# Optimization experiments

Measured on AMD Instinct MI355X. Metric: run time of the kernel, lower is better.

Reference implementation:

```python
import jax, jax.numpy as jnp
import numpy as np

EPS = 1e-6

def _layer_norm(x, w, b):
    mu = jnp.mean(x, axis=-1, keepdims=True)
    var = jnp.mean((x - mu) ** 2, axis=-1, keepdims=True)
    return (x - mu) * jax.lax.rsqrt(var + EPS) * w + b

def setup_inputs() -> dict:
    key = jax.random.key(0)
    ks = jax.random.split(key, 8)
    B, N, C = 4, 1024, 2048
    H = C * 2  # mlp hidden = 2*feature_dim
    std = 0.01
    x = jax.random.normal(ks[0], (B, N, C), dtype=jnp.float32)
    wq = jax.random.normal(ks[1], (C, C), dtype=jnp.float32) * std
    wk = jax.random.normal(ks[2], (C, C), dtype=jnp.float32) * std
    wv = jax.random.normal(ks[3], (C, C), dtype=jnp.float32) * std
    ln1_w = jnp.ones((C,), jnp.float32); ln1_b = jnp.zeros((C,), jnp.float32)
    fc1_w = jax.random.normal(ks[4], (H, C), dtype=jnp.float32) * std
    fc1_b = jnp.zeros((H,), jnp.float32)
    fc2_w = jax.random.normal(ks[5], (C, H), dtype=jnp.float32) * std
    fc2_b = jnp.zeros((C,), jnp.float32)
    ln2_w = jnp.ones((C,), jnp.float32); ln2_b = jnp.zeros((C,), jnp.float32)
    return {"x": x, "wq": wq, "wk": wk, "wv": wv,
            "ln1_w": ln1_w, "ln1_b": ln1_b,
            "fc1_w": fc1_w, "fc1_b": fc1_b,
            "fc2_w": fc2_w, "fc2_b": fc2_b,
            "ln2_w": ln2_w, "ln2_b": ln2_b}

def reference(x, wq, wk, wv, ln1_w, ln1_b, fc1_w, fc1_b, fc2_w, fc2_b, ln2_w, ln2_b):
    B, N, C = x.shape
    num_head = 32
    d = C // num_head
    # QKV projections (no bias), split heads: [B, H, N, d]
    def proj(w):
        return (x @ w.T).reshape(B, N, num_head, d).transpose(0, 2, 1, 3)
    q, k, v = proj(wq), proj(wk), proj(wv)
    scale = 1.0 / jnp.sqrt(jnp.float32(d))
    attn = jnp.einsum('bhnd,bhmd->bhnm', q * scale, k)
    attn = jax.nn.softmax(attn, axis=-1)
    out = jnp.einsum('bhnm,bhmd->bhnd', attn, v)
    out = out.transpose(0, 2, 1, 3).reshape(B, N, C)
    out = _layer_norm(out + x, ln1_w, ln1_b)
    # MLP with residual + post-LN
    h = jax.nn.relu(out @ fc1_w.T + fc1_b)
    h = h @ fc2_w.T + fc2_b
    out = _layer_norm(out + h, ln2_w, ln2_b)
    return out
```

## Files before the change

kernel.cpp:

```cpp
#include <hip/hip_runtime.h>

#define C_DIM   2048
#define H_DIM   4096
#define NSEQ    1024
#define NBATCH  4
#define BN_ROWS 4096
#define NHEAD   32
#define DHEAD   64

typedef __attribute__((ext_vector_type(8))) short  short8;
typedef __attribute__((ext_vector_type(4))) float  f32x4;

__device__ __forceinline__ float bf2f(unsigned short u) {
    union { unsigned int i; float f; } v; v.i = ((unsigned int)u) << 16; return v.f;
}
__device__ __forceinline__ unsigned short f2bf(float f) {
    union { float f; unsigned int i; } v; v.f = f;
    unsigned int r = v.i + 0x7fffu + ((v.i >> 16) & 1u);
    return (unsigned short)(r >> 16);
}

#define G2L16(gp, lp) \
    __builtin_amdgcn_global_load_lds((const __attribute__((address_space(1))) void*)(gp), \
                                     (__attribute__((address_space(3))) void*)(lp), 16, 0, 0)

__global__ __launch_bounds__(256)
void cvt_all(const float* __restrict__ x,   unsigned short* __restrict__ xo,
             const float* __restrict__ w0,  unsigned short* __restrict__ w0o,
             const float* __restrict__ w1,  unsigned short* __restrict__ w1o,
             const float* __restrict__ w2,  unsigned short* __restrict__ w2o,
             const float* __restrict__ w3,  unsigned short* __restrict__ w3o,
             const float* __restrict__ w4,  unsigned short* __restrict__ w4o)
{
    int bid = blockIdx.x;
    const float* src; unsigned short* dst;
    if      (bid < 4096)  { src = x;  dst = xo;  }
    else if (bid < 6144)  { src = w0; dst = w0o; bid -= 4096;  }
    else if (bid < 8192)  { src = w1; dst = w1o; bid -= 6144;  }
    else if (bid < 10240) { src = w2; dst = w2o; bid -= 8192;  }
    else if (bid < 14336) { src = w3; dst = w3o; bid -= 10240; }
    else                  { src = w4; dst = w4o; bid -= 14336; }
    const size_t i = ((size_t)bid * 256 + threadIdx.x) * 8;
    float4 a = *(const float4*)(src + i);
    float4 b = *(const float4*)(src + i + 4);
    unsigned short o[8] = { f2bf(a.x), f2bf(a.y), f2bf(a.z), f2bf(a.w),
                            f2bf(b.x), f2bf(b.y), f2bf(b.z), f2bf(b.w) };
    *(int4*)(dst + i) = *(const int4*)o;
}

template<int EPI, typename OUT_T>
__global__ __launch_bounds__(256)
void gemm_ring(const unsigned short* __restrict__ A,
               const unsigned short* __restrict__ B,
               const float* __restrict__ bias,
               OUT_T* __restrict__ C, int M, int N, int K)
{
    __shared__ unsigned short As[4][128 * 32];
    __shared__ unsigned short Bs[4][128 * 32];

    const int t    = threadIdx.x;
    const int lane = t & 63;
    const int wave = t >> 6;
    const int m0 = blockIdx.x * 128, n0 = blockIdx.y * 128;
    const int wm = (wave >> 1) * 64, wn = (wave & 1) * 64;
    const int lr = lane & 15;
    const int kq = lane >> 4;
    const int lrow = lane >> 2;
    const int lcol = (lane & 3) * 8;
    const int NT = K >> 5;

    const int arow = m0 + wave * 32 + lrow;
    const int brow = n0 + wave * 32 + lrow;
    const int rb   = wave * 32;

    f32x4 acc[4][4] = {};

#define STAGE_T(slot, ktile) do {                                              \
    const int koff_ = (ktile) * 32 + lcol;                                     \
    G2L16(&A[(size_t)(arow)      * K + koff_], &As[slot][ rb       * 32]);     \
    G2L16(&A[(size_t)(arow + 16) * K + koff_], &As[slot][(rb + 16) * 32]);     \
    G2L16(&B[(size_t)(brow)      * K + koff_], &Bs[slot][ rb       * 32]);     \
    G2L16(&B[(size_t)(brow + 16) * K + koff_], &Bs[slot][(rb + 16) * 32]);     \
  } while (0)

    STAGE_T(0, 0);
    STAGE_T(1, 1);
    STAGE_T(2, 2);

    for (int kt = 0; kt < NT; ++kt) {
        if (kt < NT - 2)       asm volatile("s_waitcnt vmcnt(8)" ::: "memory");
        else if (kt == NT - 2) asm volatile("s_waitcnt vmcnt(4)" ::: "memory");
        else                   asm volatile("s_waitcnt vmcnt(0)" ::: "memory");
        __builtin_amdgcn_s_barrier();

        const int s = kt & 3;
        short8 af[4], bf[4];
        #pragma unroll
        for (int i = 0; i < 4; ++i)
            af[i] = *(const short8*)&As[s][(wm + i * 16 + lr) * 32 + kq * 8];
        #pragma unroll
        for (int j = 0; j < 4; ++j)
            bf[j] = *(const short8*)&Bs[s][(wn + j * 16 + lr) * 32 + kq * 8];
        #pragma unroll
        for (int i = 0; i < 4; ++i)
            #pragma unroll
            for (int j = 0; j < 4; ++j)
                acc[i][j] = __builtin_amdgcn_mfma_f32_16x16x32_bf16(af[i], bf[j], acc[i][j], 0, 0, 0);

        if (kt + 3 < NT) STAGE_T((kt + 3) & 3, kt + 3);
    }

    #pragma unroll
    for (int j = 0; j < 4; ++j) {
        const int col = n0 + wn + j * 16 + lr;
        float bv = 0.f;
        if (EPI > 0) bv = bias[col];
        #pragma unroll
        for (int i = 0; i < 4; ++i) {
            #pragma unroll
            for (int r = 0; r < 4; ++r) {
                const int row = m0 + wm + i * 16 + kq * 4 + r;
                float v = acc[i][j][r] + bv;
                if (EPI == 1) v = fmaxf(v, 0.f);
                if constexpr (sizeof(OUT_T) == 2) C[(size_t)row * N + col] = f2bf(v);
                else                              C[(size_t)row * N + col] = v;
            }
        }
    }
#undef STAGE_T
}

__global__ __launch_bounds__(256)
void gemm_qkv(const unsigned short* __restrict__ A,
              const unsigned short* __restrict__ Wq,
              const unsigned short* __restrict__ Wk,
              const unsigned short* __restrict__ Wv,
              unsigned short* __restrict__ Qo,
              unsigned short* __restrict__ Ko,
              unsigned short* __restrict__ Vo)
{
    __shared__ unsigned short As[4][128 * 32];
    __shared__ unsigned short Bs[4][128 * 32];

    const int t    = threadIdx.x;
    const int lane = t & 63;
    const int wave = t >> 6;
    const int m0 = blockIdx.x * 128;
    const int ng = blockIdx.y * 128;
    const unsigned short* B; unsigned short* Cp; int n0;
    if      (ng < 2048) { B = Wq; Cp = Qo; n0 = ng; }
    else if (ng < 4096) { B = Wk; Cp = Ko; n0 = ng - 2048; }
    else                { B = Wv; Cp = Vo; n0 = ng - 4096; }

    const int wm = (wave >> 1) * 64, wn = (wave & 1) * 64;
    const int lr = lane & 15;
    const int kq = lane >> 4;
    const int lrow = lane >> 2;
    const int lcol = (lane & 3) * 8;
    const int NT = C_DIM >> 5;

    const int arow = m0 + wave * 32 + lrow;
    const int brow = n0 + wave * 32 + lrow;
    const int rb   = wave * 32;

    f32x4 acc[4][4] = {};

#define STAGE_T(slot, ktile) do {                                                   \
    const int koff_ = (ktile) * 32 + lcol;                                          \
    G2L16(&A[(size_t)(arow)      * C_DIM + koff_], &As[slot][ rb       * 32]);      \
    G2L16(&A[(size_t)(arow + 16) * C_DIM + koff_], &As[slot][(rb + 16) * 32]);      \
    G2L16(&B[(size_t)(brow)      * C_DIM + koff_], &Bs[slot][ rb       * 32]);      \
    G2L16(&B[(size_t)(brow + 16) * C_DIM + koff_], &Bs[slot][(rb + 16) * 32]);      \
  } while (0)

    STAGE_T(0, 0);
    STAGE_T(1, 1);
    STAGE_T(2, 2);

    for (int kt = 0; kt < NT; ++kt) {
        if (kt < NT - 2)       asm volatile("s_waitcnt vmcnt(8)" ::: "memory");
        else if (kt == NT - 2) asm volatile("s_waitcnt vmcnt(4)" ::: "memory");
        else                   asm volatile("s_waitcnt vmcnt(0)" ::: "memory");
        __builtin_amdgcn_s_barrier();

        const int s = kt & 3;
        short8 af[4], bf[4];
        #pragma unroll
        for (int i = 0; i < 4; ++i)
            af[i] = *(const short8*)&As[s][(wm + i * 16 + lr) * 32 + kq * 8];
        #pragma unroll
        for (int j = 0; j < 4; ++j)
            bf[j] = *(const short8*)&Bs[s][(wn + j * 16 + lr) * 32 + kq * 8];
        #pragma unroll
        for (int i = 0; i < 4; ++i)
            #pragma unroll
            for (int j = 0; j < 4; ++j)
                acc[i][j] = __builtin_amdgcn_mfma_f32_16x16x32_bf16(af[i], bf[j], acc[i][j], 0, 0, 0);

        if (kt + 3 < NT) STAGE_T((kt + 3) & 3, kt + 3);
    }

    #pragma unroll
    for (int j = 0; j < 4; ++j) {
        const int col = n0 + wn + j * 16 + lr;
        #pragma unroll
        for (int i = 0; i < 4; ++i) {
            #pragma unroll
            for (int r = 0; r < 4; ++r) {
                const int row = m0 + wm + i * 16 + kq * 4 + r;
                Cp[(size_t)row * C_DIM + col] = f2bf(acc[i][j][r]);
            }
        }
    }
#undef STAGE_T
}

#define LDK 72
__global__ __launch_bounds__(256)
void attn_mfma(const unsigned short* __restrict__ Qg,
               const unsigned short* __restrict__ Kg,
               const unsigned short* __restrict__ Vg,
               unsigned short* __restrict__ Og)
{
    __shared__ unsigned short Ks[64 * LDK];
    __shared__ unsigned short Vt[64 * LDK];
    __shared__ unsigned short Ps[64 * LDK];

    const int t    = threadIdx.x;
    const int lane = t & 63;
    const int wave = t >> 6;
    const int lr   = lane & 15;
    const int quad = lane >> 4;
    const int bh = blockIdx.y;
    const int b  = bh >> 5, h = bh & 31;
    const int q0 = blockIdx.x * 64;
    const int colbase = h * 64;

    short8 qf[2];
    {
        const size_t qrow = (size_t)(b * NSEQ + q0 + wave * 16 + lr) * C_DIM + colbase;
        #pragma unroll
        for (int kc = 0; kc < 2; ++kc) {
            short8 raw = *(const short8*)(Qg + qrow + kc * 32 + quad * 8);
            short8 sc;
            #pragma unroll
            for (int j = 0; j < 8; ++j)
                sc[j] = (short)f2bf(bf2f((unsigned short)raw[j]) * 0.125f);
            qf[kc] = sc;
        }
    }

    f32x4 Oacc[4] = {};
    float li[4] = {};

    for (int kt = 0; kt < 16; ++kt) {
        __syncthreads();
        {
            const int r = t >> 2, sg = (t & 3) * 16;
            const size_t grow = (size_t)(b * NSEQ + kt * 64 + r) * C_DIM + colbase + sg;
            *(int4*)&Ks[r * LDK + sg]     = *(const int4*)(Kg + grow);
            *(int4*)&Ks[r * LDK + sg + 8] = *(const int4*)(Kg + grow + 8);
        }
        {
            const int key = t & 63, d0 = (t >> 6) * 16;
            const size_t grow = (size_t)(b * NSEQ + kt * 64 + key) * C_DIM + colbase + d0;
            int4 u0 = *(const int4*)(Vg + grow);
            int4 u1 = *(const int4*)(Vg + grow + 8);
            const unsigned short* us0 = (const unsigned short*)&u0;
            const unsigned short* us1 = (const unsigned short*)&u1;
            #pragma unroll
            for (int j = 0; j < 8; ++j) {
                Vt[(d0 + j)     * LDK + key] = us0[j];
                Vt[(d0 + j + 8) * LDK + key] = us1[j];
            }
        }
        __syncthreads();

        f32x4 s[4] = {};
        #pragma unroll
        for (int n = 0; n < 4; ++n)
            #pragma unroll
            for (int kc = 0; kc < 2; ++kc) {
                short8 kf = *(const short8*)&Ks[(n * 16 + lr) * LDK + kc * 32 + quad * 8];
                s[n] = __builtin_amdgcn_mfma_f32_16x16x32_bf16(qf[kc], kf, s[n], 0, 0, 0);
            }

        float p[4][4];
        #pragma unroll
        for (int r = 0; r < 4; ++r) {
            #pragma unroll
            for (int n = 0; n < 4; ++n) { p[n][r] = __expf(s[n][r]); }
            li[r] += p[0][r] + p[1][r] + p[2][r] + p[3][r];
        }

        #pragma unroll
        for (int r = 0; r < 4; ++r)
            #pragma unroll
            for (int n = 0; n < 4; ++n)
                Ps[(wave * 16 + quad * 4 + r) * LDK + n * 16 + lr] = f2bf(p[n][r]);

        short8 pf[2];
        #pragma unroll
        for (int kc = 0; kc < 2; ++kc)
            pf[kc] = *(const short8*)&Ps[(wave * 16 + lr) * LDK + kc * 32 + quad * 8];

        #pragma unroll
        for (int n = 0; n < 4; ++n)
            #pragma unroll
            for (int kc = 0; kc < 2; ++kc) {
                short8 vf = *(const short8*)&Vt[(n * 16 + lr) * LDK + kc * 32 + quad * 8];
                Oacc[n] = __builtin_amdgcn_mfma_f32_16x16x32_bf16(pf[kc], vf, Oacc[n], 0, 0, 0);
            }
    }

    #pragma unroll
    for (int r = 0; r < 4; ++r) {
        #pragma unroll
        for (int off = 1; off < 16; off <<= 1) li[r] += __shfl_xor(li[r], off, 64);
        const float inv = 1.f / li[r];
        const size_t rowb = (size_t)(b * NSEQ + q0 + wave * 16 + quad * 4 + r) * C_DIM + colbase;
        #pragma unroll
        for (int n = 0; n < 4; ++n)
            Og[rowb + n * 16 + lr] = f2bf(Oacc[n][r] * inv);
    }
}

__global__ __launch_bounds__(256)
void ln_fused1(const unsigned short* __restrict__ a, const float* __restrict__ xr,
               const float* __restrict__ w, const float* __restrict__ bb,
               unsigned short* __restrict__ y16)
{
    const int row = blockIdx.x, t = threadIdx.x;
    const size_t base = (size_t)row * C_DIM;
    const int c0 = t * 8;
    float v[8];
    int4 ai = *(const int4*)(a + base + c0);
    const unsigned short* as = (const unsigned short*)&ai;
    float4 x0 = *(const float4*)(xr + base + c0);
    float4 x1 = *(const float4*)(xr + base + c0 + 4);
    v[0] = bf2f(as[0]) + x0.x; v[1] = bf2f(as[1]) + x0.y;
    v[2] = bf2f(as[2]) + x0.z; v[3] = bf2f(as[3]) + x0.w;
    v[4] = bf2f(as[4]) + x1.x; v[5] = bf2f(as[5]) + x1.y;
    v[6] = bf2f(as[6]) + x1.z; v[7] = bf2f(as[7]) + x1.w;

    float s = 0.f, s2 = 0.f;
    #pragma unroll
    for (int k = 0; k < 8; ++k) { s += v[k]; s2 += v[k] * v[k]; }
    #pragma unroll
    for (int off = 32; off; off >>= 1) { s += __shfl_xor(s, off, 64); s2 += __shfl_xor(s2, off, 64); }
    __shared__ float red[8];
    if ((t & 63) == 0) { red[t >> 6] = s; red[4 + (t >> 6)] = s2; }
    __syncthreads();
    s  = red[0] + red[1] + red[2] + red[3];
    s2 = red[4] + red[5] + red[6] + red[7];
    const float mu = s * (1.f / C_DIM);
    const float rs = rsqrtf(s2 * (1.f / C_DIM) - mu * mu + 1e-6f);

    float4 w0 = *(const float4*)(w + c0);
    float4 w1 = *(const float4*)(w + c0 + 4);
    float4 b0 = *(const float4*)(bb + c0);
    float4 b1 = *(const float4*)(bb + c0 + 4);
    const float* wf = (const float*)&w0; const float* wg = (const float*)&w1;
    const float* bf = (const float*)&b0; const float* bg = (const float*)&b1;
    unsigned short o16[8];
    #pragma unroll
    for (int k = 0; k < 4; ++k) {
        o16[k]     = f2bf((v[k]     - mu) * rs * wf[k] + bf[k]);
        o16[k + 4] = f2bf((v[k + 4] - mu) * rs * wg[k] + bg[k]);
    }
    *(int4*)(y16 + base + c0) = *(const int4*)o16;
}

__global__ __launch_bounds__(256)
void ln_fused2(const unsigned short* __restrict__ a, const unsigned short* __restrict__ b2,
               const float* __restrict__ w, const float* __restrict__ bb,
               float* __restrict__ out)
{
    const int row = blockIdx.x, t = threadIdx.x;
    const size_t base = (size_t)row * C_DIM;
    const int c0 = t * 8;
    float v[8];
    int4 ai = *(const int4*)(a + base + c0);
    int4 bi = *(const int4*)(b2 + base + c0);
    const unsigned short* as = (const unsigned short*)&ai;
    const unsigned short* bs = (const unsigned short*)&bi;
    #pragma unroll
    for (int k = 0; k < 8; ++k) v[k] = bf2f(as[k]) + bf2f(bs[k]);

    float s = 0.f, s2 = 0.f;
    #pragma unroll
    for (int k = 0; k < 8; ++k) { s += v[k]; s2 += v[k] * v[k]; }
    #pragma unroll
    for (int off = 32; off; off >>= 1) { s += __shfl_xor(s, off, 64); s2 += __shfl_xor(s2, off, 64); }
    __shared__ float red[8];
    if ((t & 63) == 0) { red[t >> 6] = s; red[4 + (t >> 6)] = s2; }
    __syncthreads();
    s  = red[0] + red[1] + red[2] + red[3];
    s2 = red[4] + red[5] + red[6] + red[7];
    const float mu = s * (1.f / C_DIM);
    const float rs = rsqrtf(s2 * (1.f / C_DIM) - mu * mu + 1e-6f);

    float4 w0 = *(const float4*)(w + c0);
    float4 w1 = *(const float4*)(w + c0 + 4);
    float4 b0 = *(const float4*)(bb + c0);
    float4 b1 = *(const float4*)(bb + c0 + 4);
    const float* wf = (const float*)&w0; const float* wg = (const float*)&w1;
    const float* bf = (const float*)&b0; const float* bg = (const float*)&b1;
    float4 o0, o1;
    #pragma unroll
    for (int k = 0; k < 4; ++k) {
        ((float*)&o0)[k] = (v[k]     - mu) * rs * wf[k] + bf[k];
        ((float*)&o1)[k] = (v[k + 4] - mu) * rs * wg[k] + bg[k];
    }
    *(float4*)(out + base + c0)     = o0;
    *(float4*)(out + base + c0 + 4) = o1;
}

extern "C" void kernel_launch(void* const* d_in, const int* in_sizes, int n_in,
                              void* d_out, int out_size, void* d_ws, size_t ws_size,
                              hipStream_t stream)
{
    (void)in_sizes; (void)n_in; (void)out_size; (void)ws_size;
    const float* x    = (const float*)d_in[0];
    const float* wq   = (const float*)d_in[1];
    const float* wk   = (const float*)d_in[2];
    const float* wv   = (const float*)d_in[3];
    const float* ln1w = (const float*)d_in[4];
    const float* ln1b = (const float*)d_in[5];
    const float* fc1w = (const float*)d_in[6];
    const float* fc1b = (const float*)d_in[7];
    const float* fc2w = (const float*)d_in[8];
    const float* fc2b = (const float*)d_in[9];
    const float* ln2w = (const float*)d_in[10];
    const float* ln2b = (const float*)d_in[11];

    char* ws = (char*)d_ws;
    const size_t MB16 = (size_t)BN_ROWS * C_DIM * 2;
    unsigned short* xb    = (unsigned short*)(ws);
    unsigned short* attnb = (unsigned short*)(ws);
    unsigned short* wqb   = (unsigned short*)(ws + MB16);
    unsigned short* wkb   = (unsigned short*)(ws + MB16 + MB16 / 2);
    unsigned short* y16   = (unsigned short*)(ws + MB16);
    unsigned short* wvb   = (unsigned short*)(ws + 2 * MB16);
    unsigned short* fc1wb = (unsigned short*)(ws + 2 * MB16 + MB16 / 2);
    unsigned short* fc2wb = (unsigned short*)(ws + 3 * MB16 + MB16 / 2);
    unsigned short* q_ws  = (unsigned short*)(ws + 4 * MB16 + MB16 / 2);
    unsigned short* h2    = (unsigned short*)(ws + 4 * MB16 + MB16 / 2);
    unsigned short* k_ws  = (unsigned short*)(ws + 5 * MB16 + MB16 / 2);
    unsigned short* v_ws  = (unsigned short*)(ws + 6 * MB16 + MB16 / 2);
    unsigned short* hbuf  = (unsigned short*)(ws + 5 * MB16 + MB16 / 2);

    dim3 blk(256);

    cvt_all<<<dim3(18432), blk, 0, stream>>>(x, xb, wq, wqb, wk, wkb, wv, wvb,
                                             fc1w, fc1wb, fc2w, fc2wb);

    gemm_qkv<<<dim3(32, 48), blk, 0, stream>>>(xb, wqb, wkb, wvb, q_ws, k_ws, v_ws);
    attn_mfma<<<dim3(NSEQ / 64, NBATCH * NHEAD), blk, 0, stream>>>(q_ws, k_ws, v_ws, attnb);
    ln_fused1<<<dim3(BN_ROWS), blk, 0, stream>>>(attnb, x, ln1w, ln1b, y16);
    gemm_ring<1, unsigned short><<<dim3(32, 32), blk, 0, stream>>>(y16, fc1wb, fc1b, hbuf, BN_ROWS, H_DIM, C_DIM);
    gemm_ring<2, unsigned short><<<dim3(32, 16), blk, 0, stream>>>(hbuf, fc2wb, fc2b, h2, BN_ROWS, C_DIM, H_DIM);
    ln_fused2<<<dim3(BN_ROWS), blk, 0, stream>>>(y16, h2, ln2w, ln2b, (float*)d_out);
}
```

Before: 580.9 us.

## Use 256x256-tile 8-wave GEMM with swizzled LDS for QKV and FC1

Adds a new GEMM body with 256x256 output tiles, 512 threads (8 waves), K-tile of 64, double-buffered LDS filled by direct global-to-LDS loads, and an XOR swizzle to avoid bank conflicts. It interleaves staged loads with MFMA quarter-steps and raises wave priority around the MFMA blocks. QKV and FC1 now use it instead of the 128x128 ring kernel. Larger tiles raise arithmetic intensity and cut global traffic. The costs are 128KB of LDS per block, fewer blocks (256 to 384) for 256 CUs, and many barriers per K step.

```diff
diff --git a/kernel.cpp b/kernel.cpp
--- a/kernel.cpp
+++ b/kernel.cpp
@@ -48,6 +48,167 @@
     *(int4*)(dst + i) = *(const int4*)o;
 }
 
+template<int EPI>
+__device__ __forceinline__
+void gemm256_body(const unsigned short* __restrict__ A,
+                  const unsigned short* __restrict__ B,
+                  const float* __restrict__ bias,
+                  unsigned short* __restrict__ C,
+                  const int m0, const int n0, const int K, const int ldc)
+{
+    __shared__ unsigned short As[2][256 * 64];
+    __shared__ unsigned short Bs[2][256 * 64];
+
+    const int t  = threadIdx.x;
+    const int l  = t & 63;
+    const int w  = t >> 6;
+    const int wr = w >> 2;
+    const int wc = w & 3;
+    const int lr = l & 15;
+    const int kq = l >> 4;
+    const int slotA = lr & 7;
+
+    const int sr = l >> 3;
+    const int sg = ((l & 7) ^ sr) * 8;
+
+    f32x4 acc[8][4] = {};
+    short8 bf[4][2], af[2][2];
+
+#define STG(src, srow0, ktile, ldsdst) do {                                         \
+    const unsigned short* gp0_ = (src) + (size_t)((srow0) + w * 8 + sr) * K         \
+                                  + (ktile) * 64 + sg;                              \
+    const unsigned short* gp1_ = (src) + (size_t)((srow0) + 64 + w * 8 + sr) * K    \
+                                  + (ktile) * 64 + sg;                              \
+    G2L16(gp0_, (ldsdst) + (w * 8) * 64);                                           \
+    G2L16(gp1_, (ldsdst) + (64 + w * 8) * 64);                                      \
+  } while (0)
+
+#define LDB(buf) do {                                                               \
+    _Pragma("unroll") for (int n_ = 0; n_ < 4; ++n_)                                \
+      _Pragma("unroll") for (int ks_ = 0; ks_ < 2; ++ks_)                           \
+        bf[n_][ks_] = *(const short8*)&Bs[buf][                                     \
+            (wc * 64 + n_ * 16 + lr) * 64 + (((ks_ << 2) | kq) ^ slotA) * 8];       \
+  } while (0)
+
+#define LDA(buf, q) do {                                                            \
+    _Pragma("unroll") for (int i_ = 0; i_ < 2; ++i_)                                \
+      _Pragma("unroll") for (int ks_ = 0; ks_ < 2; ++ks_)                           \
+        af[i_][ks_] = *(const short8*)&As[buf][                                     \
+            (wr * 128 + ((q) * 2 + i_) * 16 + lr) * 64                              \
+            + (((ks_ << 2) | kq) ^ slotA) * 8];                                     \
+  } while (0)
+
+#define MM(q) do {                                                                  \
+    __builtin_amdgcn_s_setprio(1);                                                  \
+    _Pragma("unroll") for (int i_ = 0; i_ < 2; ++i_)                                \
+      _Pragma("unroll") for (int n_ = 0; n_ < 4; ++n_)                              \
+        _Pragma("unroll") for (int ks_ = 0; ks_ < 2; ++ks_)                         \
+          acc[(q) * 2 + i_][n_] = __builtin_amdgcn_mfma_f32_16x16x32_bf16(          \
+              af[i_][ks_], bf[n_][ks_], acc[(q) * 2 + i_][n_], 0, 0, 0);            \
+    __builtin_amdgcn_s_setprio(0);                                                  \
+  } while (0)
+
+#define BARR() __builtin_amdgcn_s_barrier()
+#define WLG0() asm volatile("s_waitcnt lgkmcnt(0)" ::: "memory")
+
+    const int NT = K >> 6;
+    const int IT = NT >> 1;
+
+    STG(B, n0,       0, &Bs[0][0]);
+    STG(B, n0 + 128, 0, &Bs[0][128 * 64]);
+    STG(A, m0,       0, &As[0][0]);
+    STG(A, m0 + 128, 0, &As[0][128 * 64]);
+    STG(B, n0,       1, &Bs[1][0]);
+    STG(B, n0 + 128, 1, &Bs[1][128 * 64]);
+    asm volatile("s_waitcnt vmcnt(4)" ::: "memory");
+    BARR();
+
+    for (int it = 0; it < IT; ++it) {
+        const int T1 = 2 * it + 1, T2 = 2 * it + 2, T3 = 2 * it + 3;
+        const bool haveT2 = (T2 < NT), haveT3 = (T3 < NT);
+
+        LDB(0); LDA(0, 0);
+        STG(A, m0, T1, &As[1][0]);
+        BARR(); WLG0(); MM(0); BARR();
+        LDA(0, 1);
+        STG(A, m0 + 128, T1, &As[1][128 * 64]);
+        BARR(); WLG0(); MM(1); BARR();
+        LDA(0, 2);
+        if (haveT2) STG(B, n0, T2, &Bs[0][0]);
+        BARR(); WLG0(); MM(2); BARR();
+        LDA(0, 3);
+        if (haveT2) STG(B, n0 + 128, T2, &Bs[0][128 * 64]);
+        BARR(); WLG0(); MM(3);
+        if (haveT2) asm volatile("s_waitcnt vmcnt(4)" ::: "memory");
+        else        asm volatile("s_waitcnt vmcnt(0)" ::: "memory");
+        BARR();
+        LDB(1); LDA(1, 0);
+        if (haveT2) STG(A, m0, T2, &As[0][0]);
+        BARR(); WLG0(); MM(0); BARR();
+        LDA(1, 1);
+        if (haveT2) STG(A, m0 + 128, T2, &As[0][128 * 64]);
+        BARR(); WLG0(); MM(1); BARR();
+        LDA(1, 2);
+        if (haveT3) STG(B, n0, T3, &Bs[1][0]);
+        BARR(); WLG0(); MM(2); BARR();
+        LDA(1, 3);
+        if (haveT3) STG(B, n0 + 128, T3, &Bs[1][128 * 64]);
+        BARR(); WLG0(); MM(3);
+        if (it + 1 < IT) asm volatile("s_waitcnt vmcnt(4)" ::: "memory");
+        BARR();
+    }
+
+    #pragma unroll
+    for (int n = 0; n < 4; ++n) {
+        const int col = n0 + wc * 64 + n * 16 + lr;
+        float bv = 0.f;
+        if (EPI > 0) bv = bias[col];
+        #pragma unroll
+        for (int m = 0; m < 8; ++m) {
+            #pragma unroll
+            for (int r = 0; r < 4; ++r) {
+                const int row = m0 + wr * 128 + m * 16 + kq * 4 + r;
+                float v = acc[m][n][r] + bv;
+                if (EPI == 1) v = fmaxf(v, 0.f);
+                C[(size_t)row * ldc + col] = f2bf(v);
+            }
+        }
+    }
+#undef STG
+#undef LDB
+#undef LDA
+#undef MM
+#undef BARR
+#undef WLG0
+}
+
+__global__ __launch_bounds__(512, 2)
+void gemm256_fc1(const unsigned short* __restrict__ A,
+                 const unsigned short* __restrict__ B,
+                 const float* __restrict__ bias,
+                 unsigned short* __restrict__ C)
+{
+    gemm256_body<1>(A, B, bias, C, blockIdx.x * 256, blockIdx.y * 256, C_DIM, H_DIM);
+}
+
+__global__ __launch_bounds__(512, 2)
+void gemm256_qkv(const unsigned short* __restrict__ A,
+                 const unsigned short* __restrict__ Wq,
+                 const unsigned short* __restrict__ Wk,
+                 const unsigned short* __restrict__ Wv,
+                 unsigned short* __restrict__ Qo,
+                 unsigned short* __restrict__ Ko,
+                 unsigned short* __restrict__ Vo)
+{
+    const int by = blockIdx.y;
+    const unsigned short* B; unsigned short* Cp;
+    if      (by < 8)  { B = Wq; Cp = Qo; }
+    else if (by < 16) { B = Wk; Cp = Ko; }
+    else              { B = Wv; Cp = Vo; }
+    const int n0 = (by & 7) * 256;
+    gemm256_body<0>(A, B, nullptr, Cp, blockIdx.x * 256, n0, C_DIM, C_DIM);
+}
+
 template<int EPI, typename OUT_T>
 __global__ __launch_bounds__(256)
 void gemm_ring(const unsigned short* __restrict__ A,
@@ -94,18 +255,18 @@
         __builtin_amdgcn_s_barrier();
 
         const int s = kt & 3;
-        short8 af[4], bf[4];
+        short8 af[4], bfr[4];
         #pragma unroll
         for (int i = 0; i < 4; ++i)
             af[i] = *(const short8*)&As[s][(wm + i * 16 + lr) * 32 + kq * 8];
         #pragma unroll
         for (int j = 0; j < 4; ++j)
-            bf[j] = *(const short8*)&Bs[s][(wn + j * 16 + lr) * 32 + kq * 8];
+            bfr[j] = *(const short8*)&Bs[s][(wn + j * 16 + lr) * 32 + kq * 8];
         #pragma unroll
         for (int i = 0; i < 4; ++i)
             #pragma unroll
             for (int j = 0; j < 4; ++j)
-                acc[i][j] = __builtin_amdgcn_mfma_f32_16x16x32_bf16(af[i], bf[j], acc[i][j], 0, 0, 0);
+                acc[i][j] = __builtin_amdgcn_mfma_f32_16x16x32_bf16(af[i], bfr[j], acc[i][j], 0, 0, 0);
 
         if (kt + 3 < NT) STAGE_T((kt + 3) & 3, kt + 3);
     }
@@ -124,91 +285,6 @@
                 if (EPI == 1) v = fmaxf(v, 0.f);
                 if constexpr (sizeof(OUT_T) == 2) C[(size_t)row * N + col] = f2bf(v);
                 else                              C[(size_t)row * N + col] = v;
-            }
-        }
-    }
-#undef STAGE_T
-}
-
-__global__ __launch_bounds__(256)
-void gemm_qkv(const unsigned short* __restrict__ A,
-              const unsigned short* __restrict__ Wq,
-              const unsigned short* __restrict__ Wk,
-              const unsigned short* __restrict__ Wv,
-              unsigned short* __restrict__ Qo,
-              unsigned short* __restrict__ Ko,
-              unsigned short* __restrict__ Vo)
-{
-    __shared__ unsigned short As[4][128 * 32];
-    __shared__ unsigned short Bs[4][128 * 32];
-
-    const int t    = threadIdx.x;
-    const int lane = t & 63;
-    const int wave = t >> 6;
-    const int m0 = blockIdx.x * 128;
-    const int ng = blockIdx.y * 128;
-    const unsigned short* B; unsigned short* Cp; int n0;
-    if      (ng < 2048) { B = Wq; Cp = Qo; n0 = ng; }
-    else if (ng < 4096) { B = Wk; Cp = Ko; n0 = ng - 2048; }
-    else                { B = Wv; Cp = Vo; n0 = ng - 4096; }
-
-    const int wm = (wave >> 1) * 64, wn = (wave & 1) * 64;
-    const int lr = lane & 15;
-    const int kq = lane >> 4;
-    const int lrow = lane >> 2;
-    const int lcol = (lane & 3) * 8;
-    const int NT = C_DIM >> 5;
-
-    const int arow = m0 + wave * 32 + lrow;
-    const int brow = n0 + wave * 32 + lrow;
-    const int rb   = wave * 32;
-
-    f32x4 acc[4][4] = {};
-
-#define STAGE_T(slot, ktile) do {                                                   \
-    const int koff_ = (ktile) * 32 + lcol;                                          \
-    G2L16(&A[(size_t)(arow)      * C_DIM + koff_], &As[slot][ rb       * 32]);      \
-    G2L16(&A[(size_t)(arow + 16) * C_DIM + koff_], &As[slot][(rb + 16) * 32]);      \
-    G2L16(&B[(size_t)(brow)      * C_DIM + koff_], &Bs[slot][ rb       * 32]);      \
-    G2L16(&B[(size_t)(brow + 16) * C_DIM + koff_], &Bs[slot][(rb + 16) * 32]);      \
-  } while (0)
-
-    STAGE_T(0, 0);
-    STAGE_T(1, 1);
-    STAGE_T(2, 2);
-
-    for (int kt = 0; kt < NT; ++kt) {
-        if (kt < NT - 2)       asm volatile("s_waitcnt vmcnt(8)" ::: "memory");
-        else if (kt == NT - 2) asm volatile("s_waitcnt vmcnt(4)" ::: "memory");
-        else                   asm volatile("s_waitcnt vmcnt(0)" ::: "memory");
-        __builtin_amdgcn_s_barrier();
-
-        const int s = kt & 3;
-        short8 af[4], bf[4];
-        #pragma unroll
-        for (int i = 0; i < 4; ++i)
-            af[i] = *(const short8*)&As[s][(wm + i * 16 + lr) * 32 + kq * 8];
-        #pragma unroll
-        for (int j = 0; j < 4; ++j)
-            bf[j] = *(const short8*)&Bs[s][(wn + j * 16 + lr) * 32 + kq * 8];
-        #pragma unroll
-        for (int i = 0; i < 4; ++i)
-            #pragma unroll
-            for (int j = 0; j < 4; ++j)
-                acc[i][j] = __builtin_amdgcn_mfma_f32_16x16x32_bf16(af[i], bf[j], acc[i][j], 0, 0, 0);
-
-        if (kt + 3 < NT) STAGE_T((kt + 3) & 3, kt + 3);
-    }
-
-    #pragma unroll
-    for (int j = 0; j < 4; ++j) {
-        const int col = n0 + wn + j * 16 + lr;
-        #pragma unroll
-        for (int i = 0; i < 4; ++i) {
-            #pragma unroll
-            for (int r = 0; r < 4; ++r) {
-                const int row = m0 + wm + i * 16 + kq * 4 + r;
-                Cp[(size_t)row * C_DIM + col] = f2bf(acc[i][j][r]);
             }
         }
     }
@@ -256,10 +332,10 @@
     for (int kt = 0; kt < 16; ++kt) {
         __syncthreads();
         {
-            const int r = t >> 2, sg = (t & 3) * 16;
-            const size_t grow = (size_t)(b * NSEQ + kt * 64 + r) * C_DIM + colbase + sg;
-            *(int4*)&Ks[r * LDK + sg]     = *(const int4*)(Kg + grow);
-            *(int4*)&Ks[r * LDK + sg + 8] = *(const int4*)(Kg + grow + 8);
+            const int r = t >> 2, sg2 = (t & 3) * 16;
+            const size_t grow = (size_t)(b * NSEQ + kt * 64 + r) * C_DIM + colbase + sg2;
+            *(int4*)&Ks[r * LDK + sg2]     = *(const int4*)(Kg + grow);
+            *(int4*)&Ks[r * LDK + sg2 + 8] = *(const int4*)(Kg + grow + 8);
         }
         {
             const int key = t & 63, d0 = (t >> 6) * 16;
@@ -455,10 +531,10 @@
     cvt_all<<<dim3(18432), blk, 0, stream>>>(x, xb, wq, wqb, wk, wkb, wv, wvb,
                                              fc1w, fc1wb, fc2w, fc2wb);
 
-    gemm_qkv<<<dim3(32, 48), blk, 0, stream>>>(xb, wqb, wkb, wvb, q_ws, k_ws, v_ws);
+    gemm256_qkv<<<dim3(16, 24), dim3(512), 0, stream>>>(xb, wqb, wkb, wvb, q_ws, k_ws, v_ws);
     attn_mfma<<<dim3(NSEQ / 64, NBATCH * NHEAD), blk, 0, stream>>>(q_ws, k_ws, v_ws, attnb);
     ln_fused1<<<dim3(BN_ROWS), blk, 0, stream>>>(attnb, x, ln1w, ln1b, y16);
-    gemm_ring<1, unsigned short><<<dim3(32, 32), blk, 0, stream>>>(y16, fc1wb, fc1b, hbuf, BN_ROWS, H_DIM, C_DIM);
+    gemm256_fc1<<<dim3(16, 16), dim3(512), 0, stream>>>(y16, fc1wb, fc1b, hbuf);
     gemm_ring<2, unsigned short><<<dim3(32, 16), blk, 0, stream>>>(hbuf, fc2wb, fc2b, h2, BN_ROWS, C_DIM, H_DIM);
     ln_fused2<<<dim3(BN_ROWS), blk, 0, stream>>>(y16, h2, ln2w, ln2b, (float*)d_out);
 }
```

Result: no change. 588.7 us (+1.3%).

## Write V transposed from QKV GEMM and load V fragments directly in attention

Applied to the files above, without the earlier changes.

The QKV GEMM now writes V in transposed [C, B*N] layout, so the attention kernel loads V fragments straight from global memory into registers. This drops the per-tile LDS transpose of V and its scalar shared-memory stores. The QKV GEMM is also rewritten without the 4-stage ring pipeline: it uses a single LDS buffer with two syncthreads per k-tile, which exposes global-load latency. The transposed V stores are 8-byte scattered writes at large stride.

```diff
diff --git a/kernel.cpp b/kernel.cpp
--- a/kernel.cpp
+++ b/kernel.cpp
@@ -9,6 +9,7 @@
 #define DHEAD   64
 
 typedef __attribute__((ext_vector_type(8))) short  short8;
+typedef __attribute__((ext_vector_type(4))) short  short4v;
 typedef __attribute__((ext_vector_type(4))) float  f32x4;
 
 __device__ __forceinline__ float bf2f(unsigned short u) {
@@ -48,6 +49,90 @@
     *(int4*)(dst + i) = *(const int4*)o;
 }
 
+__global__ __launch_bounds__(256)
+void gemm_qkv(const unsigned short* __restrict__ A,
+              const unsigned short* __restrict__ Wq,
+              const unsigned short* __restrict__ Wk,
+              const unsigned short* __restrict__ Wv,
+              unsigned short* __restrict__ Qo,
+              unsigned short* __restrict__ Ko,
+              unsigned short* __restrict__ Vo)
+{
+    __shared__ unsigned short As[128 * 32];
+    __shared__ unsigned short Bs[128 * 32];
+
+    const int t    = threadIdx.x;
+    const int lane = t & 63;
+    const int wave = t >> 6;
+    const int m0 = blockIdx.x * 128;
+    const int ng = blockIdx.y * 128;
+    const unsigned short* B; unsigned short* Cp; int n0; bool vtrans = false;
+    if      (ng < 2048) { B = Wq; Cp = Qo; n0 = ng; }
+    else if (ng < 4096) { B = Wk; Cp = Ko; n0 = ng - 2048; }
+    else                { B = Wv; Cp = Vo; n0 = ng - 4096; vtrans = true; }
+
+    const int wm = (wave >> 1) * 64, wn = (wave & 1) * 64;
+    const int lr = lane & 15;
+    const int kq = lane >> 4;
+
+    f32x4 acc[4][4] = {};
+
+    const int lrow = lane >> 2;
+    const int lcol = (lane & 3) * 8;
+
+    for (int kt = 0; kt < C_DIM; kt += 32) {
+        __syncthreads();
+        #pragma unroll
+        for (int p = 0; p < 2; ++p) {
+            const int rb = wave * 32 + p * 16;
+            G2L16(&A[(size_t)(m0 + rb + lrow) * C_DIM + kt + lcol], &As[rb * 32]);
+            G2L16(&B[(size_t)(n0 + rb + lrow) * C_DIM + kt + lcol], &Bs[rb * 32]);
+        }
+        __syncthreads();
+
+        short8 af[4], bf[4];
+        #pragma unroll
+        for (int i = 0; i < 4; ++i)
+            af[i] = *(const short8*)&As[(wm + i * 16 + lr) * 32 + kq * 8];
+        #pragma unroll
+        for (int j = 0; j < 4; ++j)
+            bf[j] = *(const short8*)&Bs[(wn + j * 16 + lr) * 32 + kq * 8];
+        #pragma unroll
+        for (int i = 0; i < 4; ++i)
+            #pragma unroll
+            for (int j = 0; j < 4; ++j)
+                acc[i][j] = __builtin_amdgcn_mfma_f32_16x16x32_bf16(af[i], bf[j], acc[i][j], 0, 0, 0);
+    }
+
+    if (!vtrans) {
+        #pragma unroll
+        for (int j = 0; j < 4; ++j) {
+            const int col = n0 + wn + j * 16 + lr;
+            #pragma unroll
+            for (int i = 0; i < 4; ++i) {
+                #pragma unroll
+                for (int r = 0; r < 4; ++r) {
+                    const int row = m0 + wm + i * 16 + kq * 4 + r;
+                    Cp[(size_t)row * C_DIM + col] = f2bf(acc[i][j][r]);
+                }
+            }
+        }
+    } else {
+        #pragma unroll
+        for (int j = 0; j < 4; ++j) {
+            const int col = n0 + wn + j * 16 + lr;
+            #pragma unroll
+            for (int i = 0; i < 4; ++i) {
+                const int row0 = m0 + wm + i * 16 + kq * 4;
+                short4v o4;
+                #pragma unroll
+                for (int r = 0; r < 4; ++r) o4[r] = (short)f2bf(acc[i][j][r]);
+                *(short4v*)&Vo[(size_t)col * BN_ROWS + row0] = o4;
+            }
+        }
+    }
+}
+
 template<int EPI, typename OUT_T>
 __global__ __launch_bounds__(256)
 void gemm_ring(const unsigned short* __restrict__ A,
@@ -94,18 +179,18 @@
         __builtin_amdgcn_s_barrier();
 
         const int s = kt & 3;
-        short8 af[4], bf[4];
+        short8 af[4], bfr[4];
         #pragma unroll
         for (int i = 0; i < 4; ++i)
             af[i] = *(const short8*)&As[s][(wm + i * 16 + lr) * 32 + kq * 8];
         #pragma unroll
         for (int j = 0; j < 4; ++j)
-            bf[j] = *(const short8*)&Bs[s][(wn + j * 16 + lr) * 32 + kq * 8];
+            bfr[j] = *(const short8*)&Bs[s][(wn + j * 16 + lr) * 32 + kq * 8];
         #pragma unroll
         for (int i = 0; i < 4; ++i)
             #pragma unroll
             for (int j = 0; j < 4; ++j)
-                acc[i][j] = __builtin_amdgcn_mfma_f32_16x16x32_bf16(af[i], bf[j], acc[i][j], 0, 0, 0);
+                acc[i][j] = __builtin_amdgcn_mfma_f32_16x16x32_bf16(af[i], bfr[j], acc[i][j], 0, 0, 0);
 
         if (kt + 3 < NT) STAGE_T((kt + 3) & 3, kt + 3);
     }
@@ -130,100 +215,14 @@
 #undef STAGE_T
 }
 
-__global__ __launch_bounds__(256)
-void gemm_qkv(const unsigned short* __restrict__ A,
-              const unsigned short* __restrict__ Wq,
-              const unsigned short* __restrict__ Wk,
-              const unsigned short* __restrict__ Wv,
-              unsigned short* __restrict__ Qo,
-              unsigned short* __restrict__ Ko,
-              unsigned short* __restrict__ Vo)
-{
-    __shared__ unsigned short As[4][128 * 32];
-    __shared__ unsigned short Bs[4][128 * 32];
-
-    const int t    = threadIdx.x;
-    const int lane = t & 63;
-    const int wave = t >> 6;
-    const int m0 = blockIdx.x * 128;
-    const int ng = blockIdx.y * 128;
-    const unsigned short* B; unsigned short* Cp; int n0;
-    if      (ng < 2048) { B = Wq; Cp = Qo; n0 = ng; }
-    else if (ng < 4096) { B = Wk; Cp = Ko; n0 = ng - 2048; }
-    else                { B = Wv; Cp = Vo; n0 = ng - 4096; }
-
-    const int wm = (wave >> 1) * 64, wn = (wave & 1) * 64;
-    const int lr = lane & 15;
-    const int kq = lane >> 4;
-    const int lrow = lane >> 2;
-    const int lcol = (lane & 3) * 8;
-    const int NT = C_DIM >> 5;
-
-    const int arow = m0 + wave * 32 + lrow;
-    const int brow = n0 + wave * 32 + lrow;
-    const int rb   = wave * 32;
-
-    f32x4 acc[4][4] = {};
-
-#define STAGE_T(slot, ktile) do {                                                   \
-    const int koff_ = (ktile) * 32 + lcol;                                          \
-    G2L16(&A[(size_t)(arow)      * C_DIM + koff_], &As[slot][ rb       * 32]);      \
-    G2L16(&A[(size_t)(arow + 16) * C_DIM + koff_], &As[slot][(rb + 16) * 32]);      \
-    G2L16(&B[(size_t)(brow)      * C_DIM + koff_], &Bs[slot][ rb       * 32]);      \
-    G2L16(&B[(size_t)(brow + 16) * C_DIM + koff_], &Bs[slot][(rb + 16) * 32]);      \
-  } while (0)
-
-    STAGE_T(0, 0);
-    STAGE_T(1, 1);
-    STAGE_T(2, 2);
-
-    for (int kt = 0; kt < NT; ++kt) {
-        if (kt < NT - 2)       asm volatile("s_waitcnt vmcnt(8)" ::: "memory");
-        else if (kt == NT - 2) asm volatile("s_waitcnt vmcnt(4)" ::: "memory");
-        else                   asm volatile("s_waitcnt vmcnt(0)" ::: "memory");
-        __builtin_amdgcn_s_barrier();
-
-        const int s = kt & 3;
-        short8 af[4], bf[4];
-        #pragma unroll
-        for (int i = 0; i < 4; ++i)
-            af[i] = *(const short8*)&As[s][(wm + i * 16 + lr) * 32 + kq * 8];
-        #pragma unroll
-        for (int j = 0; j < 4; ++j)
-            bf[j] = *(const short8*)&Bs[s][(wn + j * 16 + lr) * 32 + kq * 8];
-        #pragma unroll
-        for (int i = 0; i < 4; ++i)
-            #pragma unroll
-            for (int j = 0; j < 4; ++j)
-                acc[i][j] = __builtin_amdgcn_mfma_f32_16x16x32_bf16(af[i], bf[j], acc[i][j], 0, 0, 0);
-
-        if (kt + 3 < NT) STAGE_T((kt + 3) & 3, kt + 3);
-    }
-
-    #pragma unroll
-    for (int j = 0; j < 4; ++j) {
-        const int col = n0 + wn + j * 16 + lr;
-        #pragma unroll
-        for (int i = 0; i < 4; ++i) {
-            #pragma unroll
-            for (int r = 0; r < 4; ++r) {
-                const int row = m0 + wm + i * 16 + kq * 4 + r;
-                Cp[(size_t)row * C_DIM + col] = f2bf(acc[i][j][r]);
-            }
-        }
-    }
-#undef STAGE_T
-}
-
 #define LDK 72
 __global__ __launch_bounds__(256)
 void attn_mfma(const unsigned short* __restrict__ Qg,
                const unsigned short* __restrict__ Kg,
-               const unsigned short* __restrict__ Vg,
+               const unsigned short* __restrict__ VTg,
                unsigned short* __restrict__ Og)
 {
     __shared__ unsigned short Ks[64 * LDK];
-    __shared__ unsigned short Vt[64 * LDK];
     __shared__ unsigned short Ps[64 * LDK];
 
     const int t    = threadIdx.x;
@@ -250,6 +249,8 @@
         }
     }
 
+    const unsigned short* vbase = VTg + (size_t)(colbase + lr) * BN_ROWS + b * NSEQ;
+
     f32x4 Oacc[4] = {};
     float li[4] = {};
 
@@ -261,20 +262,15 @@
             *(int4*)&Ks[r * LDK + sg]     = *(const int4*)(Kg + grow);
             *(int4*)&Ks[r * LDK + sg + 8] = *(const int4*)(Kg + grow + 8);
         }
-        {
-            const int key = t & 63, d0 = (t >> 6) * 16;
-            const size_t grow = (size_t)(b * NSEQ + kt * 64 + key) * C_DIM + colbase + d0;
-            int4 u0 = *(const int4*)(Vg + grow);
-            int4 u1 = *(const int4*)(Vg + grow + 8);
-            const unsigned short* us0 = (const unsigned short*)&u0;
-            const unsigned short* us1 = (const unsigned short*)&u1;
-            #pragma unroll
-            for (int j = 0; j < 8; ++j) {
-                Vt[(d0 + j)     * LDK + key] = us0[j];
-                Vt[(d0 + j + 8) * LDK + key] = us1[j];
-            }
-        }
         __syncthreads();
+
+        short8 vf[4][2];
+        #pragma unroll
+        for (int n = 0; n < 4; ++n)
+            #pragma unroll
+            for (int kc = 0; kc < 2; ++kc)
+                vf[n][kc] = *(const short8*)(vbase + (size_t)(n * 16) * BN_ROWS
+                                             + kt * 64 + kc * 32 + quad * 8);
 
         f32x4 s[4] = {};
         #pragma unroll
@@ -307,10 +303,8 @@
         #pragma unroll
         for (int n = 0; n < 4; ++n)
             #pragma unroll
-            for (int kc = 0; kc < 2; ++kc) {
-                short8 vf = *(const short8*)&Vt[(n * 16 + lr) * LDK + kc * 32 + quad * 8];
-                Oacc[n] = __builtin_amdgcn_mfma_f32_16x16x32_bf16(pf[kc], vf, Oacc[n], 0, 0, 0);
-            }
+            for (int kc = 0; kc < 2; ++kc)
+                Oacc[n] = __builtin_amdgcn_mfma_f32_16x16x32_bf16(pf[kc], vf[n][kc], Oacc[n], 0, 0, 0);
     }
 
     #pragma unroll
```

Measured after the change: 732.6 us. +26.1%, slower.
